# Kernel optimization log

Hardware: AMD Instinct MI355X
Metric: run time of the kernel (lower is better)

The kernel has to match this reference:

```python
import jax, jax.numpy as jnp
import numpy as np

B, N, IN_F, OUT_F = 32, 1024, 256, 256
ALPHA = 0.2  # LeakyReLU negative slope
NEG_INF = -9e15  # matches torch's -9000000000000000.0 masking constant


def setup_inputs() -> dict:
    key = jax.random.key(0)
    k1, k2, k3, k4 = jax.random.split(key, 4)
    h = jax.random.normal(k1, (B, N, IN_F), dtype=jnp.float32)
    adj = jax.random.randint(k2, (B, N, N), 0, 2, dtype=jnp.int32)
    W = jax.random.normal(k3, (OUT_F, IN_F), dtype=jnp.float32) * 0.05
    a = jax.random.normal(k4, (1, 2 * OUT_F), dtype=jnp.float32) * 0.05
    return {"h": h, "adj": adj, "W": W, "a": a}


def reference(h, adj, W, a):
    # Wh: (B, N, out)
    Wh = jnp.einsum("bni,oi->bno", h, W)
    # Decompose a([Wh_i || Wh_j]) = Wh_i . a1 + Wh_j . a2 (identical math,
    # avoids the O(B*N^2*2*out) concat intermediate of the torch code).
    a1 = a[0, :OUT_F]   # (out,)
    a2 = a[0, OUT_F:]   # (out,)
    si = Wh @ a1        # (B, N) score contribution of source node i
    sj = Wh @ a2        # (B, N) score contribution of neighbor node j
    e = jax.nn.leaky_relu(si[:, :, None] + sj[:, None, :], negative_slope=ALPHA)
    attention = jnp.where(adj > 0, e, NEG_INF)
    attention = jax.nn.softmax(attention, axis=-1)
    # dropout omitted (eval mode)
    h_prime = jnp.einsum("bij,bjo->bio", attention, Wh)
    return jax.nn.elu(h_prime)
```

## Files before the change

kernel.cpp:

```cpp
#include <hip/hip_runtime.h>
#include <hip/hip_bf16.h>


#define ALPHA 0.2f
#define LOG2E 1.44269504f

typedef __bf16 bf16x8 __attribute__((ext_vector_type(8)));
typedef __bf16 bf16x4 __attribute__((ext_vector_type(4)));
typedef float  f32x4  __attribute__((ext_vector_type(4)));
typedef unsigned long long u64;

__global__ __launch_bounds__(256) void k1_gemm1(const float* __restrict__ h,
                                                const float* __restrict__ W,
                                                const float* __restrict__ a_g,
                                                __bf16* __restrict__ whT,
                                                float* __restrict__ si,
                                                float* __restrict__ sj) {
    __shared__ __bf16 hA[64 * 72];
    __shared__ __bf16 hB[256 * 72];
    __shared__ float  red[512];
    const int t    = threadIdx.x;
    const int r0   = blockIdx.x * 64;
    const int b    = r0 >> 10;
    const int n0   = r0 & 1023;
    const int w    = t >> 6;
    const int l    = t & 63;
    const int ln   = l & 15;
    const int quad = l >> 4;

    f32x4 acc[4][4] = {};
    float4 ha_r[4], wb_r[16];

    #pragma unroll
    for (int it = 0; it < 4; ++it)
        ha_r[it] = *(const float4*)&h[(size_t)(r0 + it * 16 + (t >> 4)) * 256 + (t & 15) * 4];
    #pragma unroll
    for (int it = 0; it < 16; ++it)
        wb_r[it] = *(const float4*)&W[(size_t)(it * 16 + (t >> 4)) * 256 + (t & 15) * 4];

    for (int kc = 0; kc < 4; ++kc) {
        #pragma unroll
        for (int it = 0; it < 4; ++it) {
            const float4 v = ha_r[it];
            bf16x4 pv = {(__bf16)v.x, (__bf16)v.y, (__bf16)v.z, (__bf16)v.w};
            *(bf16x4*)&hA[(it * 16 + (t >> 4)) * 72 + (t & 15) * 4] = pv;
        }
        #pragma unroll
        for (int it = 0; it < 16; ++it) {
            const float4 v = wb_r[it];
            bf16x4 pv = {(__bf16)v.x, (__bf16)v.y, (__bf16)v.z, (__bf16)v.w};
            *(bf16x4*)&hB[(it * 16 + (t >> 4)) * 72 + (t & 15) * 4] = pv;
        }
        __syncthreads();
        if (kc < 3) {
            const int k0 = (kc + 1) * 64;
            #pragma unroll
            for (int it = 0; it < 4; ++it)
                ha_r[it] = *(const float4*)&h[(size_t)(r0 + it * 16 + (t >> 4)) * 256 + k0 + (t & 15) * 4];
            #pragma unroll
            for (int it = 0; it < 16; ++it)
                wb_r[it] = *(const float4*)&W[(size_t)(it * 16 + (t >> 4)) * 256 + k0 + (t & 15) * 4];
        }
        #pragma unroll
        for (int kk = 0; kk < 2; ++kk) {
            bf16x8 af[4], bfr[4];
            #pragma unroll
            for (int ri = 0; ri < 4; ++ri)
                af[ri] = *(const bf16x8*)&hA[(ri * 16 + ln) * 72 + kk * 32 + quad * 8];
            #pragma unroll
            for (int oi = 0; oi < 4; ++oi)
                bfr[oi] = *(const bf16x8*)&hB[(w * 64 + oi * 16 + ln) * 72 + kk * 32 + quad * 8];
            #pragma unroll
            for (int ri = 0; ri < 4; ++ri)
                #pragma unroll
                for (int oi = 0; oi < 4; ++oi)
                    acc[ri][oi] = __builtin_amdgcn_mfma_f32_16x16x32_bf16(
                        af[ri], bfr[oi], acc[ri][oi], 0, 0, 0);
        }
        __syncthreads();
    }

    #pragma unroll
    for (int ri = 0; ri < 4; ++ri) {
        const int n = ri * 16 + quad * 4;
        #pragma unroll
        for (int oi = 0; oi < 4; ++oi) {
            const int o = w * 64 + oi * 16 + ln;
            bf16x4 pv = {(__bf16)acc[ri][oi][0], (__bf16)acc[ri][oi][1],
                         (__bf16)acc[ri][oi][2], (__bf16)acc[ri][oi][3]};
            *(bf16x4*)&hB[o * 72 + n] = pv;
        }
    }
    __syncthreads();

    #pragma unroll
    for (int it = 0; it < 8; ++it) {
        const int o   = w * 64 + it * 8 + (l >> 3);
        const int seg = l & 7;
        const bf16x8 v = *(const bf16x8*)&hB[o * 72 + seg * 8];
        *(bf16x8*)&whT[((size_t)b * 256 + o) * 1024 + n0 + seg * 8] = v;
    }

    {
        float s1 = 0.f, s2 = 0.f;
        #pragma unroll 8
        for (int oi = 0; oi < 64; ++oi) {
            const int o = w * 64 + oi;
            const float v = (float)hB[o * 72 + l];
            s1 += v * a_g[o];
            s2 += v * a_g[256 + o];
        }
        red[w * 64 + l]       = s1;
        red[256 + w * 64 + l] = s2;
    }
    __syncthreads();
    if (t < 64) {
        si[b * 1024 + n0 + t] =
            (red[t] + red[64 + t] + red[128 + t] + red[192 + t]) * LOG2E;
    } else if (t < 128) {
        const int n = t - 64;
        sj[b * 1024 + n0 + n] =
            (red[256 + n] + red[320 + n] + red[384 + n] + red[448 + n]) * LOG2E;
    }
}

#define K3_BODY(JC, ACUR, SJCUR, ANXT, SJNXT, SBUF)                                    \
  {                                                                                    \
    const int j0 = (JC) * 64;                                                          \
             \
    bf16x8 bfr[2][4];                                                                  \
    _Pragma("unroll")                                                                  \
    for (int kk = 0; kk < 2; ++kk)                                                     \
      _Pragma("unroll")                                                                \
      for (int oi = 0; oi < 4; ++oi)                                                   \
        bfr[kk][oi] = *(const bf16x8*)&whTb[                                           \
            (size_t)(w * 64 + oi * 16 + ln) * 1024 + j0 + kk * 32 + quad * 8];         \
            \
    if ((JC) < 15) {                                                                   \
      _Pragma("unroll")                                                                \
      for (int m = 0; m < 2; ++m)                                                      \
        ANXT[m] = *(const int4*)&adjb[(size_t)(m * 16 + g) * 1024 + j0 + 64 + j4 * 4]; \
      SJNXT = *(const float4*)&sj_g[b * 1024 + j0 + 64 + j4 * 4];                      \
    }                                                                                  \
                \
    _Pragma("unroll")                                                                  \
    for (int m = 0; m < 2; ++m) {                                                      \
      const int il = m * 16 + g;                                                       \
      float e0 = si_r[m] + SJCUR.x; e0 = e0 > 0.f ? e0 : ALPHA * e0;                   \
      float e1 = si_r[m] + SJCUR.y; e1 = e1 > 0.f ? e1 : ALPHA * e1;                   \
      float e2 = si_r[m] + SJCUR.z; e2 = e2 > 0.f ? e2 : ALPHA * e2;                   \
      float e3 = si_r[m] + SJCUR.w; e3 = e3 > 0.f ? e3 : ALPHA * e3;                   \
      const float w0 = ACUR[m].x > 0 ? exp2f(e0) : 0.f;                                \
      const float w1 = ACUR[m].y > 0 ? exp2f(e1) : 0.f;                                \
      const float w2 = ACUR[m].z > 0 ? exp2f(e2) : 0.f;                                \
      const float w3 = ACUR[m].w > 0 ? exp2f(e3) : 0.f;                                \
      bf16x4 pv = {(__bf16)w0, (__bf16)w1, (__bf16)w2, (__bf16)w3};                    \
      dsum[m] += (float)pv[0] + (float)pv[1] + (float)pv[2] + (float)pv[3];            \
      *(bf16x4*)&SBUF[il * 72 + j4 * 4] = pv;                                          \
    }                                                                                  \
    __syncthreads();                                                                   \
                         \
    _Pragma("unroll")                                                                  \
    for (int kk = 0; kk < 2; ++kk) {                                                   \
      bf16x8 af[2];                                                                    \
      _Pragma("unroll")                                                                \
      for (int ri = 0; ri < 2; ++ri)                                                   \
        af[ri] = *(const bf16x8*)&SBUF[(ri * 16 + ln) * 72 + kk * 32 + quad * 8];      \
      _Pragma("unroll")                                                                \
      for (int ri = 0; ri < 2; ++ri)                                                   \
        _Pragma("unroll")                                                              \
        for (int oi = 0; oi < 4; ++oi)                                                 \
          acc[ri][oi] = __builtin_amdgcn_mfma_f32_16x16x32_bf16(                       \
              af[ri], bfr[kk][oi], acc[ri][oi], 0, 0, 0);                              \
    }                                                                                  \
             \
                                   \
  }

__global__ __launch_bounds__(256, 4) void k3_attn(const int* __restrict__ adj,
                                                  const __bf16* __restrict__ whT,
                                                  const float* __restrict__ si_g,
                                                  const float* __restrict__ sj_g,
                                                  float* __restrict__ out) {
    __shared__ __bf16 lds_s0[32 * 72];
    __shared__ __bf16 lds_s1[32 * 72];
    __shared__ float  lds_denom[32];
    const int t = threadIdx.x;
    const int orig = blockIdx.x;
    const int wgid = (orig & 7) * 128 + (orig >> 3);
    const int b    = wgid >> 5;
    const int i0   = (wgid & 31) << 5;
    const int w    = t >> 6;
    const int l    = t & 63;
    const int ln   = l & 15;
    const int quad = l >> 4;
    const int g    = t >> 4;
    const int j4   = t & 15;

    float si_r[2];
    #pragma unroll
    for (int m = 0; m < 2; ++m) si_r[m] = si_g[b * 1024 + i0 + m * 16 + g];

    float dsum[2] = {0.f, 0.f};
    f32x4 acc[2][4] = {};
    const __bf16* whTb = whT + (size_t)b * 256 * 1024;
    const int*    adjb = adj + ((size_t)(b * 1024 + i0)) * 1024;

    int4   a_c[2], a_n[2];
    float4 sj_c, sj_n;
    #pragma unroll
    for (int m = 0; m < 2; ++m)
        a_c[m] = *(const int4*)&adjb[(size_t)(m * 16 + g) * 1024 + j4 * 4];
    sj_c = *(const float4*)&sj_g[b * 1024 + j4 * 4];

    for (int jj = 0; jj < 8; ++jj) {
        K3_BODY(2 * jj,     a_c, sj_c, a_n, sj_n, lds_s0);
        K3_BODY(2 * jj + 1, a_n, sj_n, a_c, sj_c, lds_s1);
    }

    #pragma unroll
    for (int m = 0; m < 2; ++m) {
        float v = dsum[m];
        v += __shfl_xor(v, 1);
        v += __shfl_xor(v, 2);
        v += __shfl_xor(v, 4);
        v += __shfl_xor(v, 8);
        if (j4 == 0) lds_denom[m * 16 + g] = v;
    }
    __syncthreads();
    #pragma unroll
    for (int ri = 0; ri < 2; ++ri) {
        #pragma unroll
        for (int q = 0; q < 4; ++q) {
            const int il = ri * 16 + quad * 4 + q;
            const float dinv = 1.0f / fmaxf(lds_denom[il], 1e-30f);
            #pragma unroll
            for (int oi = 0; oi < 4; ++oi) {
                const int o = w * 64 + oi * 16 + ln;
                const float v = acc[ri][oi][q] * dinv;
                const float r = v > 0.f ? v : __expf(v) - 1.f;
                out[((size_t)(b * 1024 + i0 + il)) * 256 + o] = r;
            }
        }
    }
}

extern "C" void kernel_launch(void* const* d_in, const int* in_sizes, int n_in,
                              void* d_out, int out_size, void* d_ws, size_t ws_size,
                              hipStream_t stream) {
    const float* h   = (const float*)d_in[0];
    const int*   adj = (const int*)d_in[1];
    const float* W   = (const float*)d_in[2];
    const float* a   = (const float*)d_in[3];
    float* out = (float*)d_out;

    __bf16* whT = (__bf16*)d_ws;
    float*  si  = (float*)((char*)d_ws + (size_t)16777216);
    float*  sj  = (float*)((char*)d_ws + (size_t)16777216 + 131072);

    k1_gemm1<<<512, 256, 0, stream>>>(h, W, a, whT, si, sj);
    k3_attn<<<1024, 256, 0, stream>>>(adj, whT, si, sj, out);
}
```

Measured before the change: 302.1 us.

## Double attention row tile to 64 rows and prefetch adjacency two chunks ahead

```diff
diff --git a/kernel.cpp b/kernel.cpp
--- a/kernel.cpp
+++ b/kernel.cpp
@@ -124,10 +124,11 @@
     }
 }
 
-#define K3_BODY(JC, ACUR, SJCUR, ANXT, SJNXT, SBUF)                                    \
+#define K3_BODY(JC, A, SJ, SBUF)                                                       \
   {                                                                                    \
     const int j0 = (JC) * 64;                                                          \
-             \
+            \
+                              \
     bf16x8 bfr[2][4];                                                                  \
     _Pragma("unroll")                                                                  \
     for (int kk = 0; kk < 2; ++kk)                                                     \
@@ -135,61 +136,66 @@
       for (int oi = 0; oi < 4; ++oi)                                                   \
         bfr[kk][oi] = *(const bf16x8*)&whTb[                                           \
             (size_t)(w * 64 + oi * 16 + ln) * 1024 + j0 + kk * 32 + quad * 8];         \
-            \
-    if ((JC) < 15) {                                                                   \
-      _Pragma("unroll")                                                                \
-      for (int m = 0; m < 2; ++m)                                                      \
-        ANXT[m] = *(const int4*)&adjb[(size_t)(m * 16 + g) * 1024 + j0 + 64 + j4 * 4]; \
-      SJNXT = *(const float4*)&sj_g[b * 1024 + j0 + 64 + j4 * 4];                      \
-    }                                                                                  \
                 \
     _Pragma("unroll")                                                                  \
-    for (int m = 0; m < 2; ++m) {                                                      \
+    for (int m = 0; m < 4; ++m) {                                                      \
       const int il = m * 16 + g;                                                       \
-      float e0 = si_r[m] + SJCUR.x; e0 = e0 > 0.f ? e0 : ALPHA * e0;                   \
-      float e1 = si_r[m] + SJCUR.y; e1 = e1 > 0.f ? e1 : ALPHA * e1;                   \
-      float e2 = si_r[m] + SJCUR.z; e2 = e2 > 0.f ? e2 : ALPHA * e2;                   \
-      float e3 = si_r[m] + SJCUR.w; e3 = e3 > 0.f ? e3 : ALPHA * e3;                   \
-      const float w0 = ACUR[m].x > 0 ? exp2f(e0) : 0.f;                                \
-      const float w1 = ACUR[m].y > 0 ? exp2f(e1) : 0.f;                                \
-      const float w2 = ACUR[m].z > 0 ? exp2f(e2) : 0.f;                                \
-      const float w3 = ACUR[m].w > 0 ? exp2f(e3) : 0.f;                                \
+      float e0 = si_r[m] + SJ.x; e0 = e0 > 0.f ? e0 : ALPHA * e0;                      \
+      float e1 = si_r[m] + SJ.y; e1 = e1 > 0.f ? e1 : ALPHA * e1;                      \
+      float e2 = si_r[m] + SJ.z; e2 = e2 > 0.f ? e2 : ALPHA * e2;                      \
+      float e3 = si_r[m] + SJ.w; e3 = e3 > 0.f ? e3 : ALPHA * e3;                      \
+      const float w0 = A[m].x > 0 ? exp2f(e0) : 0.f;                                   \
+      const float w1 = A[m].y > 0 ? exp2f(e1) : 0.f;                                   \
+      const float w2 = A[m].z > 0 ? exp2f(e2) : 0.f;                                   \
+      const float w3 = A[m].w > 0 ? exp2f(e3) : 0.f;                                   \
       bf16x4 pv = {(__bf16)w0, (__bf16)w1, (__bf16)w2, (__bf16)w3};                    \
       dsum[m] += (float)pv[0] + (float)pv[1] + (float)pv[2] + (float)pv[3];            \
       *(bf16x4*)&SBUF[il * 72 + j4 * 4] = pv;                                          \
     }                                                                                  \
-    __syncthreads();                                                                   \
-                         \
+           \
+                            \
+    if ((JC) + 2 < 16) {                                                               \
+      _Pragma("unroll")                                                                \
+      for (int m = 0; m < 4; ++m)                                                      \
+        A[m] = *(const int4*)&adjb[(size_t)(m * 16 + g) * 1024 + j0 + 128 + j4 * 4];   \
+      SJ = *(const float4*)&sj_g[b * 1024 + j0 + 128 + j4 * 4];                        \
+    }                                                                                  \
+                               \
+    asm volatile("s_waitcnt lgkmcnt(0)");                                              \
+    __builtin_amdgcn_s_barrier();                                                      \
+                 \
+    __builtin_amdgcn_s_setprio(1);                                                     \
     _Pragma("unroll")                                                                  \
     for (int kk = 0; kk < 2; ++kk) {                                                   \
-      bf16x8 af[2];                                                                    \
-      _Pragma("unroll")                                                                \
-      for (int ri = 0; ri < 2; ++ri)                                                   \
+      bf16x8 af[4];                                                                    \
+      _Pragma("unroll")                                                                \
+      for (int ri = 0; ri < 4; ++ri)                                                   \
         af[ri] = *(const bf16x8*)&SBUF[(ri * 16 + ln) * 72 + kk * 32 + quad * 8];      \
       _Pragma("unroll")                                                                \
-      for (int ri = 0; ri < 2; ++ri)                                                   \
+      for (int ri = 0; ri < 4; ++ri)                                                   \
         _Pragma("unroll")                                                              \
         for (int oi = 0; oi < 4; ++oi)                                                 \
           acc[ri][oi] = __builtin_amdgcn_mfma_f32_16x16x32_bf16(                       \
               af[ri], bfr[kk][oi], acc[ri][oi], 0, 0, 0);                              \
     }                                                                                  \
-             \
-                                   \
+    __builtin_amdgcn_s_setprio(0);                                                     \
+              \
+                   \
   }
 
-__global__ __launch_bounds__(256, 4) void k3_attn(const int* __restrict__ adj,
+__global__ __launch_bounds__(256, 2) void k3_attn(const int* __restrict__ adj,
                                                   const __bf16* __restrict__ whT,
                                                   const float* __restrict__ si_g,
                                                   const float* __restrict__ sj_g,
                                                   float* __restrict__ out) {
-    __shared__ __bf16 lds_s0[32 * 72];
-    __shared__ __bf16 lds_s1[32 * 72];
-    __shared__ float  lds_denom[32];
+    __shared__ __bf16 lds_s0[64 * 72];
+    __shared__ __bf16 lds_s1[64 * 72];
+    __shared__ float  lds_denom[64];
     const int t = threadIdx.x;
     const int orig = blockIdx.x;
-    const int wgid = (orig & 7) * 128 + (orig >> 3);
-    const int b    = wgid >> 5;
-    const int i0   = (wgid & 31) << 5;
+    const int wgid = (orig & 7) * 64 + (orig >> 3);
+    const int b    = wgid >> 4;
+    const int i0   = (wgid & 15) << 6;
     const int w    = t >> 6;
     const int l    = t & 63;
     const int ln   = l & 15;
@@ -197,29 +203,33 @@
     const int g    = t >> 4;
     const int j4   = t & 15;
 
-    float si_r[2];
-    #pragma unroll
-    for (int m = 0; m < 2; ++m) si_r[m] = si_g[b * 1024 + i0 + m * 16 + g];
-
-    float dsum[2] = {0.f, 0.f};
-    f32x4 acc[2][4] = {};
+    float si_r[4];
+    #pragma unroll
+    for (int m = 0; m < 4; ++m) si_r[m] = si_g[b * 1024 + i0 + m * 16 + g];
+
+    float dsum[4] = {0.f, 0.f, 0.f, 0.f};
+    f32x4 acc[4][4] = {};
     const __bf16* whTb = whT + (size_t)b * 256 * 1024;
     const int*    adjb = adj + ((size_t)(b * 1024 + i0)) * 1024;
 
-    int4   a_c[2], a_n[2];
+    int4   a_c[4], a_n[4];
     float4 sj_c, sj_n;
     #pragma unroll
-    for (int m = 0; m < 2; ++m)
+    for (int m = 0; m < 4; ++m)
         a_c[m] = *(const int4*)&adjb[(size_t)(m * 16 + g) * 1024 + j4 * 4];
     sj_c = *(const float4*)&sj_g[b * 1024 + j4 * 4];
+    #pragma unroll
+    for (int m = 0; m < 4; ++m)
+        a_n[m] = *(const int4*)&adjb[(size_t)(m * 16 + g) * 1024 + 64 + j4 * 4];
+    sj_n = *(const float4*)&sj_g[b * 1024 + 64 + j4 * 4];
 
     for (int jj = 0; jj < 8; ++jj) {
-        K3_BODY(2 * jj,     a_c, sj_c, a_n, sj_n, lds_s0);
-        K3_BODY(2 * jj + 1, a_n, sj_n, a_c, sj_c, lds_s1);
-    }
-
-    #pragma unroll
-    for (int m = 0; m < 2; ++m) {
+        K3_BODY(2 * jj,     a_c, sj_c, lds_s0);
+        K3_BODY(2 * jj + 1, a_n, sj_n, lds_s1);
+    }
+
+    #pragma unroll
+    for (int m = 0; m < 4; ++m) {
         float v = dsum[m];
         v += __shfl_xor(v, 1);
         v += __shfl_xor(v, 2);
@@ -229,7 +239,7 @@
     }
     __syncthreads();
     #pragma unroll
-    for (int ri = 0; ri < 2; ++ri) {
+    for (int ri = 0; ri < 4; ++ri) {
         #pragma unroll
         for (int q = 0; q < 4; ++q) {
             const int il = ri * 16 + quad * 4 + q;
@@ -259,5 +269,5 @@
     float*  sj  = (float*)((char*)d_ws + (size_t)16777216 + 131072);
 
     k1_gemm1<<<512, 256, 0, stream>>>(h, W, a, whT, si, sj);
-    k3_attn<<<1024, 256, 0, stream>>>(adj, whT, si, sj, out);
+    k3_attn<<<512, 256, 0, stream>>>(adj, whT, si, sj, out);
 }
```

Result: faster. 256.7 us (-15.0%).
